# Kernel optimization log

Measured on AMD Instinct MI355X. Metric: run time of the kernel, lower is better.

## Reference

```python
import jax, jax.numpy as jnp
import numpy as np

VOCAB = 32000
H_EMB = 128
TOTAL_SUBTOKENS = 1_000_000
N_NODES = 200_000
PAD_IDX = 0  # nn.Embedding(padding_idx=pad) keeps that row zero


def setup_inputs() -> dict:
    key = jax.random.key(0)
    k1, k2, k3 = jax.random.split(key, 3)
    table = jax.random.normal(k1, (VOCAB, H_EMB), dtype=jnp.float32)
    table = table.at[PAD_IDX].set(0.0)  # padding row is zeros
    subtoken_ids = jax.random.randint(k2, (TOTAL_SUBTOKENS,), 0, VOCAB, dtype=jnp.int64)
    # sorted segment ids emulate contiguous per-node slices of the concatenated subtoken list
    segment_ids = jnp.sort(jax.random.randint(k3, (TOTAL_SUBTOKENS,), 0, N_NODES, dtype=jnp.int64))
    return {
        "subtoken_table": table,
        "subtoken_ids": subtoken_ids,
        "segment_ids": segment_ids,
        "n_nodes": N_NODES,
    }


def reference(subtoken_table, subtoken_ids, segment_ids, n_nodes):
    # fused embedding gather + per-node ragged sum pooling
    # [total_subtokens, h_emb] gather, then segment-sum to [n_nodes, h_emb]
    subtoken_embeds = subtoken_table[subtoken_ids]
    token_embeds = jax.ops.segment_sum(
        subtoken_embeds, segment_ids, num_segments=n_nodes,
        indices_are_sorted=True,
    )
    return token_embeds
```

## Files before the change

### kernel.cpp

```cpp
#include <hip/hip_runtime.h>


#define H_EMB   128
#define LPG     16
#define SPG     4
#define UNROLL  8
#define ROW_U4  16

__device__ __forceinline__ unsigned f2bf_rne(float f) {
    unsigned u = __float_as_uint(f);
    return (u + 0x7FFFu + ((u >> 16) & 1u)) >> 16;
}

__global__ __launch_bounds__(256)
void prep_kernel(const float* __restrict__ t, unsigned* __restrict__ ct, int n_pairs,
                 const int* __restrict__ segs, int* __restrict__ starts,
                 int n, int n_nodes)
{
    const int i = blockIdx.x * blockDim.x + threadIdx.x;
    if (i < n_pairs) {
        const float2 f = reinterpret_cast<const float2*>(t)[i];
        ct[i] = f2bf_rne(f.x) | (f2bf_rne(f.y) << 16);
    }
    if (i < n) {
        const int s  = segs[i];
        const int sp = (i == 0) ? -1 : segs[i - 1];
        for (int seg = sp + 1; seg <= s; ++seg) starts[seg] = i;
        if (i == n - 1)
            for (int seg = s + 1; seg <= n_nodes; ++seg) starts[seg] = n;
    }
}

__global__ __launch_bounds__(256)
void SubTokenEmbedding_6734508720780_kernel(
    const uint4* __restrict__ ctab,
    const int*   __restrict__ ids,
    const int*   __restrict__ segs,
    const int*   __restrict__ starts,
    float*       __restrict__ out,
    int n_nodes)
{
    const int group = (int)((blockIdx.x * blockDim.x + threadIdx.x) / LPG);
    const int lane  = (int)(threadIdx.x & (LPG - 1));
    const int s0    = group * SPG;
    if (s0 >= n_nodes) return;
    const int s_end = min(s0 + SPG, n_nodes);

    const int beg = starts[s0];
    const int end = starts[s_end];

    const uint4* trow = ctab + lane;
    float*       orow = out  + (size_t)lane * 8;

    float acc[8] = {0.f, 0.f, 0.f, 0.f, 0.f, 0.f, 0.f, 0.f};
    int cur = s0;

    int sv = 0, iv = 0;
    if (beg + lane < end) { sv = segs[beg + lane]; iv = ids[beg + lane]; }

    for (int base = beg; base < end; base += LPG) {
        const int cnt = min(LPG, end - base);
        const int nb  = base + LPG;
        int sv2 = 0, iv2 = 0;
        if (nb + lane < end) { sv2 = segs[nb + lane]; iv2 = ids[nb + lane]; }

        for (int k = 0; k < cnt; k += UNROLL) {
            int s_a[UNROLL], id_a[UNROLL];
            #pragma unroll
            for (int u = 0; u < UNROLL; ++u) {
                s_a[u]  = __shfl(sv, k + u, LPG);
                id_a[u] = __shfl(iv, k + u, LPG);
            }
            uint4 t[UNROLL];
            #pragma unroll
            for (int u = 0; u < UNROLL; ++u)
                t[u] = trow[(size_t)id_a[u] * ROW_U4];

            #pragma unroll
            for (int u = 0; u < UNROLL; ++u) {
                if (k + u < cnt) {
                    const int s = s_a[u];
                    if (s != cur) {
                        float4* o = reinterpret_cast<float4*>(orow + (size_t)cur * H_EMB);
                        o[0] = make_float4(acc[0], acc[1], acc[2], acc[3]);
                        o[1] = make_float4(acc[4], acc[5], acc[6], acc[7]);
                        #pragma unroll
                        for (int e = 0; e < 8; ++e) acc[e] = 0.f;
                        const float4 zero = make_float4(0.f, 0.f, 0.f, 0.f);
                        for (int z = cur + 1; z < s; ++z) {
                            float4* oz = reinterpret_cast<float4*>(orow + (size_t)z * H_EMB);
                            oz[0] = zero; oz[1] = zero;
                        }
                        cur = s;
                    }
                    acc[0] += __uint_as_float(t[u].x << 16);
                    acc[1] += __uint_as_float(t[u].x & 0xFFFF0000u);
                    acc[2] += __uint_as_float(t[u].y << 16);
                    acc[3] += __uint_as_float(t[u].y & 0xFFFF0000u);
                    acc[4] += __uint_as_float(t[u].z << 16);
                    acc[5] += __uint_as_float(t[u].z & 0xFFFF0000u);
                    acc[6] += __uint_as_float(t[u].w << 16);
                    acc[7] += __uint_as_float(t[u].w & 0xFFFF0000u);
                }
            }
        }
        sv = sv2; iv = iv2;
    }

    {
        float4* o = reinterpret_cast<float4*>(orow + (size_t)cur * H_EMB);
        o[0] = make_float4(acc[0], acc[1], acc[2], acc[3]);
        o[1] = make_float4(acc[4], acc[5], acc[6], acc[7]);
        const float4 zero = make_float4(0.f, 0.f, 0.f, 0.f);
        for (int z = cur + 1; z < s_end; ++z) {
            float4* oz = reinterpret_cast<float4*>(orow + (size_t)z * H_EMB);
            oz[0] = zero; oz[1] = zero;
        }
    }
}

__global__ __launch_bounds__(256)
void subtok_f32_kernel(
    const float* __restrict__ table,
    const int*   __restrict__ ids,
    const int*   __restrict__ segs,
    float*       __restrict__ out,
    int total_subtokens, int n_nodes)
{
    const int group = (int)((blockIdx.x * blockDim.x + threadIdx.x) / 32);
    const int lane  = (int)(threadIdx.x & 31);
    const int s0    = group * SPG;
    if (s0 >= n_nodes) return;
    const int s_end = min(s0 + SPG, n_nodes);

    auto lower_bound = [&](int v) -> int {
        int lo = 0, hi = total_subtokens;
        while (lo < hi) { int m = (lo + hi) >> 1; if (segs[m] < v) lo = m + 1; else hi = m; }
        return lo;
    };
    const int beg = lower_bound(s0);
    const int end = lower_bound(s_end);

    const float* trow = table + (size_t)lane * 4;
    float*       orow = out   + (size_t)lane * 4;
    float4 acc = make_float4(0.f, 0.f, 0.f, 0.f);
    int cur = s0;

    for (int j = beg; j < end; ++j) {
        const int s  = segs[j];
        const int id = ids[j];
        if (s != cur) {
            *reinterpret_cast<float4*>(orow + (size_t)cur * H_EMB) = acc;
            const float4 zero = make_float4(0.f, 0.f, 0.f, 0.f);
            for (int z = cur + 1; z < s; ++z)
                *reinterpret_cast<float4*>(orow + (size_t)z * H_EMB) = zero;
            acc = zero; cur = s;
        }
        const float4 t = *reinterpret_cast<const float4*>(trow + (size_t)id * H_EMB);
        acc.x += t.x; acc.y += t.y; acc.z += t.z; acc.w += t.w;
    }
    *reinterpret_cast<float4*>(orow + (size_t)cur * H_EMB) = acc;
    const float4 zero = make_float4(0.f, 0.f, 0.f, 0.f);
    for (int z = cur + 1; z < s_end; ++z)
        *reinterpret_cast<float4*>(orow + (size_t)z * H_EMB) = zero;
}

extern "C" void kernel_launch(void* const* d_in, const int* in_sizes, int n_in,
                              void* d_out, int out_size, void* d_ws, size_t ws_size,
                              hipStream_t stream) {
    const float* table = (const float*)d_in[0];
    const int*   ids   = (const int*)d_in[1];
    const int*   segs  = (const int*)d_in[2];
    float*       out   = (float*)d_out;

    const int total_subtokens = in_sizes[1];
    const int vocab           = in_sizes[0] / H_EMB;
    const int n_nodes         = out_size / H_EMB;

    const size_t starts_bytes = ((size_t)(n_nodes + 1) * sizeof(int) + 15) & ~(size_t)15;
    const size_t ctab_bytes   = (size_t)vocab * (H_EMB / 2) * sizeof(unsigned);
    const int    n_pairs      = vocab * (H_EMB / 2);

    if (ws_size >= starts_bytes + ctab_bytes) {
        int*      starts = (int*)d_ws;
        unsigned* ctab   = (unsigned*)((char*)d_ws + starts_bytes);

        const int prep_n = max(n_pairs, total_subtokens);
        prep_kernel<<<(prep_n + 255) / 256, 256, 0, stream>>>(
            table, ctab, n_pairs, segs, starts, total_subtokens, n_nodes);

        const int n_groups         = (n_nodes + SPG - 1) / SPG;
        const int groups_per_block = 256 / LPG;
        const int n_blocks         = (n_groups + groups_per_block - 1) / groups_per_block;
        SubTokenEmbedding_6734508720780_kernel<<<n_blocks, 256, 0, stream>>>(
            (const uint4*)ctab, ids, segs, starts, out, n_nodes);
    } else {
        const int n_groups         = (n_nodes + SPG - 1) / SPG;
        const int groups_per_block = 256 / 32;
        const int n_blocks         = (n_groups + groups_per_block - 1) / groups_per_block;
        subtok_f32_kernel<<<n_blocks, 256, 0, stream>>>(
            table, ids, segs, out, total_subtokens, n_nodes);
    }
}
```

Measured before the change: 66.56 us.

## Map one full wavefront per node group with scalar readlane index broadcast

Switches the main kernel from 16-lane groups each loading a uint4 (8 bf16) per row to a full 64-lane wavefront where each lane loads one 32-bit word (2 bf16). Segment and id values are broadcast with readlane instead of shuffles, so the indices become wave-uniform and row addresses can be computed with scalar registers. Each wave covers 8 nodes, with an unroll of 16 to keep more loads in flight. The aim is to drop shuffle overhead and improve gather coalescing, but it relies on wave64 for readlane and issues four times as many narrower load instructions per row.

After: 66.05 us. No clear change (-0.8%).

```diff
diff --git a/kernel.cpp b/kernel.cpp
--- a/kernel.cpp
+++ b/kernel.cpp
@@ -2,10 +2,9 @@
 
 
 #define H_EMB   128
-#define LPG     16
-#define SPG     4
-#define UNROLL  8
-#define ROW_U4  16
+#define SPG     8
+#define UNROLL  16
+#define ROW_U1  64
 
 __device__ __forceinline__ unsigned f2bf_rne(float f) {
     unsigned u = __float_as_uint(f);
@@ -33,34 +32,34 @@
 
 __global__ __launch_bounds__(256)
 void SubTokenEmbedding_6734508720780_kernel(
-    const uint4* __restrict__ ctab,
-    const int*   __restrict__ ids,
-    const int*   __restrict__ segs,
-    const int*   __restrict__ starts,
-    float*       __restrict__ out,
+    const unsigned* __restrict__ ctab,
+    const int*      __restrict__ ids,
+    const int*      __restrict__ segs,
+    const int*      __restrict__ starts,
+    float*          __restrict__ out,
     int n_nodes)
 {
-    const int group = (int)((blockIdx.x * blockDim.x + threadIdx.x) / LPG);
-    const int lane  = (int)(threadIdx.x & (LPG - 1));
-    const int s0    = group * SPG;
+    const int wave = (int)((blockIdx.x * blockDim.x + threadIdx.x) >> 6);
+    const int lane = (int)(threadIdx.x & 63);
+    const int s0   = wave * SPG;
     if (s0 >= n_nodes) return;
     const int s_end = min(s0 + SPG, n_nodes);
 
     const int beg = starts[s0];
     const int end = starts[s_end];
 
-    const uint4* trow = ctab + lane;
-    float*       orow = out  + (size_t)lane * 8;
+    const unsigned* trow = ctab + lane;
+    float*          orow = out  + lane * 2;
 
-    float acc[8] = {0.f, 0.f, 0.f, 0.f, 0.f, 0.f, 0.f, 0.f};
+    float accx = 0.f, accy = 0.f;
     int cur = s0;
 
     int sv = 0, iv = 0;
     if (beg + lane < end) { sv = segs[beg + lane]; iv = ids[beg + lane]; }
 
-    for (int base = beg; base < end; base += LPG) {
-        const int cnt = min(LPG, end - base);
-        const int nb  = base + LPG;
+    for (int base = beg; base < end; base += 64) {
+        const int cnt = min(64, end - base);
+        const int nb  = base + 64;
         int sv2 = 0, iv2 = 0;
         if (nb + lane < end) { sv2 = segs[nb + lane]; iv2 = ids[nb + lane]; }
 
@@ -68,55 +67,38 @@
             int s_a[UNROLL], id_a[UNROLL];
             #pragma unroll
             for (int u = 0; u < UNROLL; ++u) {
-                s_a[u]  = __shfl(sv, k + u, LPG);
-                id_a[u] = __shfl(iv, k + u, LPG);
+                s_a[u]  = __builtin_amdgcn_readlane(sv, k + u);
+                id_a[u] = __builtin_amdgcn_readlane(iv, k + u);
             }
-            uint4 t[UNROLL];
+            unsigned tv[UNROLL];
             #pragma unroll
             for (int u = 0; u < UNROLL; ++u)
-                t[u] = trow[(size_t)id_a[u] * ROW_U4];
+                tv[u] = trow[(size_t)id_a[u] * ROW_U1];
 
             #pragma unroll
             for (int u = 0; u < UNROLL; ++u) {
                 if (k + u < cnt) {
                     const int s = s_a[u];
                     if (s != cur) {
-                        float4* o = reinterpret_cast<float4*>(orow + (size_t)cur * H_EMB);
-                        o[0] = make_float4(acc[0], acc[1], acc[2], acc[3]);
-                        o[1] = make_float4(acc[4], acc[5], acc[6], acc[7]);
-                        #pragma unroll
-                        for (int e = 0; e < 8; ++e) acc[e] = 0.f;
-                        const float4 zero = make_float4(0.f, 0.f, 0.f, 0.f);
-                        for (int z = cur + 1; z < s; ++z) {
-                            float4* oz = reinterpret_cast<float4*>(orow + (size_t)z * H_EMB);
-                            oz[0] = zero; oz[1] = zero;
-                        }
+                        *reinterpret_cast<float2*>(orow + (size_t)cur * H_EMB) =
+                            make_float2(accx, accy);
+                        accx = 0.f; accy = 0.f;
+                        for (int z = cur + 1; z < s; ++z)
+                            *reinterpret_cast<float2*>(orow + (size_t)z * H_EMB) =
+                                make_float2(0.f, 0.f);
                         cur = s;
                     }
-                    acc[0] += __uint_as_float(t[u].x << 16);
-                    acc[1] += __uint_as_float(t[u].x & 0xFFFF0000u);
-                    acc[2] += __uint_as_float(t[u].y << 16);
-                    acc[3] += __uint_as_float(t[u].y & 0xFFFF0000u);
-                    acc[4] += __uint_as_float(t[u].z << 16);
-                    acc[5] += __uint_as_float(t[u].z & 0xFFFF0000u);
-                    acc[6] += __uint_as_float(t[u].w << 16);
-                    acc[7] += __uint_as_float(t[u].w & 0xFFFF0000u);
+                    accx += __uint_as_float(tv[u] << 16);
+                    accy += __uint_as_float(tv[u] & 0xFFFF0000u);
                 }
             }
         }
         sv = sv2; iv = iv2;
     }
 
-    {
-        float4* o = reinterpret_cast<float4*>(orow + (size_t)cur * H_EMB);
-        o[0] = make_float4(acc[0], acc[1], acc[2], acc[3]);
-        o[1] = make_float4(acc[4], acc[5], acc[6], acc[7]);
-        const float4 zero = make_float4(0.f, 0.f, 0.f, 0.f);
-        for (int z = cur + 1; z < s_end; ++z) {
-            float4* oz = reinterpret_cast<float4*>(orow + (size_t)z * H_EMB);
-            oz[0] = zero; oz[1] = zero;
-        }
-    }
+    *reinterpret_cast<float2*>(orow + (size_t)cur * H_EMB) = make_float2(accx, accy);
+    for (int z = cur + 1; z < s_end; ++z)
+        *reinterpret_cast<float2*>(orow + (size_t)z * H_EMB) = make_float2(0.f, 0.f);
 }
 
 __global__ __launch_bounds__(256)
@@ -189,15 +171,13 @@
         prep_kernel<<<(prep_n + 255) / 256, 256, 0, stream>>>(
             table, ctab, n_pairs, segs, starts, total_subtokens, n_nodes);
 
-        const int n_groups         = (n_nodes + SPG - 1) / SPG;
-        const int groups_per_block = 256 / LPG;
-        const int n_blocks         = (n_groups + groups_per_block - 1) / groups_per_block;
+        const int n_waves  = (n_nodes + SPG - 1) / SPG;
+        const int n_blocks = (n_waves + 3) / 4;
         SubTokenEmbedding_6734508720780_kernel<<<n_blocks, 256, 0, stream>>>(
-            (const uint4*)ctab, ids, segs, starts, out, n_nodes);
+            ctab, ids, segs, starts, out, n_nodes);
     } else {
-        const int n_groups         = (n_nodes + SPG - 1) / SPG;
-        const int groups_per_block = 256 / 32;
-        const int n_blocks         = (n_groups + groups_per_block - 1) / groups_per_block;
+        const int n_groups = (n_nodes + SPG - 1) / SPG;
+        const int n_blocks = (n_groups + 7) / 8;
         subtok_f32_kernel<<<n_blocks, 256, 0, stream>>>(
             table, ids, segs, out, total_subtokens, n_nodes);
     }
```
